# Performance work log

Measured on AMD Instinct MI355X. Metric: run time of the kernel, lower is better.

Reference implementation:

```python
import jax, jax.numpy as jnp
import numpy as np

EPS = 1e-05


def setup_inputs() -> dict:
    key = jax.random.key(0)
    k0, k1, k2, k3, k4 = jax.random.split(key, 5)
    B, N, D = 8, 4096, 1024
    scale = 1.0 / np.sqrt(D)  # roughly xavier scale for D x D
    return {
        "x": jax.random.normal(k0, (B, N, D), dtype=jnp.float32),
        "w_query_real": jax.random.normal(k1, (D, D), dtype=jnp.float32) * scale,
        "w_query_imag": jax.random.normal(k2, (D, D), dtype=jnp.float32) * scale,
        "w_key": jax.random.normal(k3, (D, D), dtype=jnp.float32) * scale,
        "w_value": jax.random.normal(k4, (D, D), dtype=jnp.float32) * scale,
    }


def reference(x, w_query_real, w_query_imag, w_key, w_value):
    # x is real -> x_real = x_imag = x (torch fallback branch)
    q_real = jnp.einsum('bnd,de->bne', x, w_query_real)
    q_imag = jnp.einsum('bnd,de->bne', x, w_query_imag)
    query = jax.nn.relu(q_real) * jax.nn.relu(q_imag)  # relu gating; dropout p=0

    key = jnp.einsum('bnd,de->bne', x, w_key)
    value = jnp.einsum('bnd,de->bne', x, w_value)
    # L2 norm over the sequence axis (dim=1), keepdim
    key = key / (jnp.linalg.norm(key, axis=1, keepdims=True) + EPS)
    value = value / (jnp.linalg.norm(value, axis=1, keepdims=True) + EPS)

    kv_attn = jax.nn.relu(jnp.einsum('bnd,bne->bde', key, value))  # [B, D, D]
    return jnp.einsum('bnd,bde->bne', query, kv_attn)
```

## Files before the change

### kernel.cpp

```cpp
#include <hip/hip_runtime.h>
#include <stdint.h>
#include <stddef.h>

#define D_ 1024
#define NSEQ_ 4096
#define BATCH_ 8
#define BN_ (BATCH_ * NSEQ_)

typedef __attribute__((ext_vector_type(8))) short short8;
typedef __attribute__((ext_vector_type(4))) short short4_t;
typedef __attribute__((ext_vector_type(4))) float float4_t;

__device__ __forceinline__ short f2b(float f) {
  union { float f; uint32_t u; } x; x.f = f;
  uint32_t r = x.u + 0x7fffu + ((x.u >> 16) & 1u);
  return (short)(r >> 16);
}
__device__ __forceinline__ float b2f(short s) {
  union { float f; uint32_t u; } x; x.u = ((uint32_t)(uint16_t)s) << 16; return x.f;
}

__device__ __forceinline__ void gll16(const void* g, void* l) {
  auto gp = reinterpret_cast<const uint32_t __attribute__((address_space(1)))*>(
      reinterpret_cast<uintptr_t>(g));
  auto lp = reinterpret_cast<uint32_t __attribute__((address_space(3)))*>(
      reinterpret_cast<uintptr_t>(l));
  __builtin_amdgcn_global_load_lds(gp, lp, 16, 0, 0);
}

#define MFMA16(a, b, c) __builtin_amdgcn_mfma_f32_16x16x32_bf16(a, b, c, 0, 0, 0)

__global__ void convert_x(const float* __restrict__ X, short* __restrict__ Xb) {
  const size_t i = (size_t)blockIdx.x * 256 + threadIdx.x;
  const float4_t* p = (const float4_t*)(X + i * 8);
  float4_t a = __builtin_nontemporal_load(p);
  float4_t b = __builtin_nontemporal_load(p + 1);
  short8 o;
  o[0] = f2b(a.x); o[1] = f2b(a.y); o[2] = f2b(a.z); o[3] = f2b(a.w);
  o[4] = f2b(b.x); o[5] = f2b(b.y); o[6] = f2b(b.z); o[7] = f2b(b.w);
  *(short8*)(Xb + i * 8) = o;
}

__global__ void transpose_convert_w(const float* __restrict__ w0, const float* __restrict__ w1,
                                    const float* __restrict__ w2, const float* __restrict__ w3,
                                    short* __restrict__ wT) {
  __shared__ float tile[32][33];
  const int z = blockIdx.z;
  const float* src = (z == 0) ? w0 : (z == 1) ? w1 : (z == 2) ? w2 : w3;
  const int d0 = blockIdx.y * 32, e0 = blockIdx.x * 32;
  const int tx = threadIdx.x, ty = threadIdx.y;
#pragma unroll
  for (int i = 0; i < 4; ++i) {
    int d = ty + i * 8;
    tile[d][tx] = __builtin_nontemporal_load(&src[(size_t)(d0 + d) * D_ + (e0 + tx)]);
  }
  __syncthreads();
#pragma unroll
  for (int i = 0; i < 4; ++i) {
    int e = ty + i * 8;
    const int eg = e0 + e;
    const int row = ((eg >> 4) << 6) + (z << 4) + (eg & 15);
    wT[(size_t)row * D_ + (d0 + tx)] = f2b(tile[tx][e]);
  }
}

__global__ __launch_bounds__(512, 2) void gemm_x4w(
    const short* __restrict__ Xb, const short* __restrict__ Wint,
    short* __restrict__ qout, short* __restrict__ kT, short* __restrict__ vT,
    float* __restrict__ ssk, float* __restrict__ ssv) {
  __shared__ short ring[4 * 16384];

  const int t = threadIdx.x;
  const int w = t >> 6;
  const int lane = t & 63;
  const int l16 = lane & 15;
  const int quad = lane >> 4;
  const int wm = w >> 2;
  const int wn = w & 3;

  const int bid = blockIdx.x;
  const int c = bid & 7;
  const int j = bid >> 3;
  const int ch = j >> 5;
  const int mtl = (ch & 1) * 8 + (j & 7);
  const int ntl = (ch >> 1) * 4 + ((j >> 3) & 3);
  const int mt = c * 16 + mtl;
  const int nt = ntl;
  const int M0 = mt * 256;
  const int N0 = nt * 256;
  const int E0 = nt * 64;

  const float4_t fz = {0.f, 0.f, 0.f, 0.f};
  float4_t acc[8][4];
#pragma unroll
  for (int i = 0; i < 8; ++i)
#pragma unroll
    for (int j2 = 0; j2 < 4; ++j2) acc[i][j2] = fz;

  size_t goffA[2], goffB[2];
  int ldsu[2];
#pragma unroll
  for (int r = 0; r < 2; ++r) {
    const int uu = w * 2 + r;
    const int row = uu * 16 + (lane >> 2);
    const int sp = (lane & 3) ^ ((row >> 1) & 3);
    goffA[r] = (size_t)(M0 + row) * 1024 + sp * 8;
    goffB[r] = (size_t)(N0 + row) * 1024 + sp * 8;
    ldsu[r] = uu * 512;
  }
  int aoff[8], boff[4];
#pragma unroll
  for (int i = 0; i < 8; ++i) {
    const int row = wm * 128 + i * 16 + l16;
    aoff[i] = row * 32 + ((quad ^ ((row >> 1) & 3)) << 3);
  }
#pragma unroll
  for (int j2 = 0; j2 < 4; ++j2) {
    const int row = wn * 64 + j2 * 16 + l16;
    boff[j2] = row * 32 + ((quad ^ ((row >> 1) & 3)) << 3);
  }

#pragma unroll
  for (int r = 0; r < 2; ++r) gll16(Xb + goffA[r], ring + ldsu[r]);
#pragma unroll
  for (int r = 0; r < 2; ++r) gll16(Wint + goffB[r], ring + 8192 + ldsu[r]);
#pragma unroll
  for (int r = 0; r < 2; ++r) gll16(Xb + goffA[r] + 32, ring + 16384 + ldsu[r]);
#pragma unroll
  for (int r = 0; r < 2; ++r) gll16(Wint + goffB[r] + 32, ring + 16384 + 8192 + ldsu[r]);
  asm volatile("s_waitcnt vmcnt(4)" ::: "memory");
  __builtin_amdgcn_s_barrier();

#pragma unroll 1
  for (int tt = 0; tt < 32; ++tt) {
    const short* As = ring + (tt & 3) * 16384;
    const short* Bs = As + 8192;
    short8 aF[8], bF[4];

#pragma unroll
    for (int i = 0; i < 4; ++i) aF[i] = *(const short8*)&As[aoff[i]];
#pragma unroll
    for (int j2 = 0; j2 < 4; ++j2) bF[j2] = *(const short8*)&Bs[boff[j2]];
    if (tt < 30) {
      short* dA = ring + ((tt + 2) & 3) * 16384;
      const int k0 = (tt + 2) * 32;
#pragma unroll
      for (int r = 0; r < 2; ++r) gll16(Xb + goffA[r] + k0, dA + ldsu[r]);
    }
    __builtin_amdgcn_s_barrier();
    asm volatile("s_waitcnt lgkmcnt(0)" ::: "memory");
    __builtin_amdgcn_s_setprio(1);
#pragma unroll
    for (int i = 0; i < 4; ++i)
#pragma unroll
      for (int j2 = 0; j2 < 4; ++j2) acc[i][j2] = MFMA16(aF[i], bF[j2], acc[i][j2]);
    __builtin_amdgcn_s_setprio(0);
    __builtin_amdgcn_s_barrier();

#pragma unroll
    for (int i = 4; i < 8; ++i) aF[i] = *(const short8*)&As[aoff[i]];
    if (tt < 30) {
      short* dB = ring + ((tt + 2) & 3) * 16384 + 8192;
      const int k0 = (tt + 2) * 32;
#pragma unroll
      for (int r = 0; r < 2; ++r) gll16(Wint + goffB[r] + k0, dB + ldsu[r]);
    }
    __builtin_amdgcn_s_barrier();
    asm volatile("s_waitcnt lgkmcnt(0)" ::: "memory");
    __builtin_amdgcn_s_setprio(1);
#pragma unroll
    for (int i = 4; i < 8; ++i)
#pragma unroll
      for (int j2 = 0; j2 < 4; ++j2) acc[i][j2] = MFMA16(aF[i], bF[j2], acc[i][j2]);
    __builtin_amdgcn_s_setprio(0);
    if (tt < 30) {
      asm volatile("s_waitcnt vmcnt(4)" ::: "memory");
    } else if (tt == 30) {
      asm volatile("s_waitcnt vmcnt(0)" ::: "memory");
    }
    __builtin_amdgcn_s_barrier();
  }

  const int e = E0 + wn * 16 + l16;
#pragma unroll
  for (int i = 0; i < 8; ++i) {
    const int rowg = M0 + wm * 128 + i * 16 + quad * 4;
#pragma unroll
    for (int rr = 0; rr < 4; ++rr) {
      float v = fmaxf(acc[i][0][rr], 0.f) * fmaxf(acc[i][1][rr], 0.f);
      qout[(size_t)(rowg + rr) * 1024 + e] = f2b(v);
    }
  }

  short* T = ring;
  const int b = M0 >> 12;
  const int n0 = M0 & 4095;
#pragma unroll
  for (int wt = 2; wt < 4; ++wt) {
    short* dst = (wt == 2) ? kT : vT;
    float* ss = (wt == 2) ? ssk : ssv;
    __syncthreads();
#pragma unroll
    for (int i = 0; i < 8; ++i) {
      const int nl = wm * 128 + i * 16 + quad * 4;
      const int el = wn * 16 + l16;
      short4_t pk;
#pragma unroll
      for (int rr = 0; rr < 4; ++rr) pk[rr] = f2b(acc[i][wt][rr]);
      *(short4_t*)&T[el * 264 + nl] = pk;
    }
    __syncthreads();
#pragma unroll
    for (int it = 0; it < 4; ++it) {
      const int ee = it * 16 + (t >> 5);
      const int nch = (t & 31) * 8;
      short8 vv = *(const short8*)&T[ee * 264 + nch];
      *(short8*)&dst[((size_t)b * 1024 + E0 + ee) * 4096 + n0 + nch] = vv;
      float s = 0.f;
#pragma unroll
      for (int x2 = 0; x2 < 8; ++x2) { float f = b2f(vv[x2]); s += f * f; }
      s += __shfl_xor(s, 1, 32);
      s += __shfl_xor(s, 2, 32);
      s += __shfl_xor(s, 4, 32);
      s += __shfl_xor(s, 8, 32);
      s += __shfl_xor(s, 16, 32);
      if ((t & 31) == 0) atomicAdd(&ss[b * 1024 + E0 + ee], s);
    }
  }
}

__global__ void finish_norms(const float* __restrict__ ss, float* __restrict__ inv) {
  const int i = blockIdx.x * 256 + threadIdx.x;
  if (i < 2 * BATCH_ * D_) inv[i] = 1.f / (sqrtf(ss[i]) + 1e-5f);
}

__global__ __launch_bounds__(256, 2) void gemm_bt(
    const short* __restrict__ A, const short* __restrict__ Bm,
    size_t sAb, size_t sBb, int K, int mode,
    const float* __restrict__ rsb, const float* __restrict__ csb,
    void* __restrict__ outp) {
  __shared__ short As[128 * 32];
  __shared__ short Bs[128 * 32];
  const int t = threadIdx.x;
  const int w = t >> 6;
  const int lane = t & 63;
  const int l16 = lane & 15;
  const int quad = lane >> 4;
  const int wm = w >> 1, wn = w & 1;
  const int M0 = blockIdx.y * 128, N0 = blockIdx.x * 128, b = blockIdx.z;
  const short* Ab = A + (size_t)b * sAb;
  const short* Bb = Bm + (size_t)b * sBb;

  const float4_t fz = {0.f, 0.f, 0.f, 0.f};
  float4_t acc[4][4];
#pragma unroll
  for (int i = 0; i < 4; ++i)
#pragma unroll
    for (int j = 0; j < 4; ++j) acc[i][j] = fz;

  const int rowq = lane >> 2;
  const int chunk = (lane & 3) * 8;

  for (int k0 = 0; k0 < K; k0 += 32) {
#pragma unroll
    for (int r = 0; r < 4; ++r) {
      const int q = w * 4 + r;
      if (q < 8) {
        const int row = q * 16 + rowq;
        gll16(Ab + (size_t)(M0 + row) * K + (k0 + chunk), &As[q * 512]);
      } else {
        const int row = (q - 8) * 16 + rowq;
        gll16(Bb + (size_t)(N0 + row) * K + (k0 + chunk), &Bs[(q - 8) * 512]);
      }
    }
    __syncthreads();
    short8 aF[4], bF[4];
#pragma unroll
    for (int i = 0; i < 4; ++i)
      aF[i] = *(const short8*)&As[(wm * 64 + i * 16 + l16) * 32 + quad * 8];
#pragma unroll
    for (int j = 0; j < 4; ++j)
      bF[j] = *(const short8*)&Bs[(wn * 64 + j * 16 + l16) * 32 + quad * 8];
#pragma unroll
    for (int i = 0; i < 4; ++i)
#pragma unroll
      for (int j = 0; j < 4; ++j) acc[i][j] = MFMA16(aF[i], bF[j], acc[i][j]);
    __syncthreads();
  }

  if (mode == 0) {
    short* ob = (short*)outp + (size_t)b * D_ * D_;
    const float* rs = rsb + b * D_ + M0;
    const float* cs = csb + b * D_ + N0;
#pragma unroll
    for (int i = 0; i < 4; ++i) {
      const int rl = wm * 64 + i * 16 + quad * 4;
#pragma unroll
      for (int j = 0; j < 4; ++j) {
        const int cl = wn * 64 + j * 16 + l16;
        const float csc = cs[cl];
#pragma unroll
        for (int rr = 0; rr < 4; ++rr) {
          float v = acc[i][j][rr] * rs[rl + rr] * csc;
          v = fmaxf(v, 0.f);
          ob[(size_t)(M0 + rl + rr) * 1024 + (N0 + cl)] = f2b(v);
        }
      }
    }
  } else {
    float* of = (float*)outp + (size_t)b * NSEQ_ * D_;
#pragma unroll
    for (int i = 0; i < 4; ++i) {
      const int rl = wm * 64 + i * 16 + quad * 4;
#pragma unroll
      for (int j = 0; j < 4; ++j) {
        const int cl = wn * 64 + j * 16 + l16;
#pragma unroll
        for (int rr = 0; rr < 4; ++rr)
          __builtin_nontemporal_store(acc[i][j][rr],
                                      &of[(size_t)(M0 + rl + rr) * 1024 + (N0 + cl)]);
      }
    }
  }
}

extern "C" void kernel_launch(void* const* d_in, const int* in_sizes, int n_in,
                              void* d_out, int out_size, void* d_ws, size_t ws_size,
                              hipStream_t stream) {
  const float* x = (const float*)d_in[0];
  const float* wqr = (const float*)d_in[1];
  const float* wqi = (const float*)d_in[2];
  const float* wk = (const float*)d_in[3];
  const float* wv = (const float*)d_in[4];

  short* wT = (short*)d_ws;
  short* qb = wT + (size_t)4 * D_ * D_;
  short* kT = qb + (size_t)BN_ * D_;
  short* vT = kT + (size_t)BATCH_ * D_ * NSEQ_;
  short* kvT = vT + (size_t)BATCH_ * D_ * NSEQ_;
  float* ssk = (float*)(kvT + (size_t)BATCH_ * D_ * D_);
  float* ssv = ssk + BATCH_ * D_;
  float* invk = ssv + BATCH_ * D_;
  float* invv = invk + BATCH_ * D_;

  short* xb = (short*)d_out;

  hipMemsetAsync(ssk, 0, (size_t)2 * BATCH_ * D_ * sizeof(float), stream);

  convert_x<<<dim3(16384), 256, 0, stream>>>(x, xb);

  transpose_convert_w<<<dim3(32, 32, 4), dim3(32, 8), 0, stream>>>(wqr, wqi, wk, wv, wT);

  gemm_x4w<<<dim3(2048), 512, 0, stream>>>(xb, wT, qb, kT, vT, ssk, ssv);

  finish_norms<<<dim3(64), 256, 0, stream>>>(ssk, invk);

  gemm_bt<<<dim3(8, 8, 8), 256, 0, stream>>>(
      vT, kT, (size_t)D_ * NSEQ_, (size_t)D_ * NSEQ_, 4096, 0, invv, invk, (void*)kvT);

  gemm_bt<<<dim3(8, 32, 8), 256, 0, stream>>>(
      qb, kvT, (size_t)NSEQ_ * D_, (size_t)D_ * D_, 1024, 1, nullptr, nullptr, d_out);
}
```

Before: 727.6 us.

## Pipeline batched GEMMs with a 4-stage LDS ring, swizzle and wider tiles

Replaces the simple synchronous gemm_bt with gemm_bt_p, which uses 512 threads and 128x256 tiles. It prefetches two K-steps ahead through a 4-buffer LDS ring with XOR swizzling, explicit vmcnt waits and s_setprio around the MFMAs. It also simplifies the block-to-tile mapping in gemm_x4w. The aim is to hide global load latency and LDS bank conflicts in the kv and output GEMMs. The cost is more LDS per block and more complex synchronisation. The tile remapping may also change L2 locality.

```diff
diff --git a/kernel.cpp b/kernel.cpp
--- a/kernel.cpp
+++ b/kernel.cpp
@@ -79,13 +79,9 @@
   const int wn = w & 3;
 
   const int bid = blockIdx.x;
-  const int c = bid & 7;
-  const int j = bid >> 3;
-  const int ch = j >> 5;
-  const int mtl = (ch & 1) * 8 + (j & 7);
-  const int ntl = (ch >> 1) * 4 + ((j >> 3) & 3);
-  const int mt = c * 16 + mtl;
-  const int nt = ntl;
+  const int lin = (bid & 7) * 256 + (bid >> 3);
+  const int mt = lin >> 4;
+  const int nt = lin & 15;
   const int M0 = mt * 256;
   const int N0 = nt * 256;
   const int E0 = nt * 64;
@@ -234,22 +230,24 @@
   if (i < 2 * BATCH_ * D_) inv[i] = 1.f / (sqrtf(ss[i]) + 1e-5f);
 }
 
-__global__ __launch_bounds__(256, 2) void gemm_bt(
+__global__ __launch_bounds__(512, 2) void gemm_bt_p(
     const short* __restrict__ A, const short* __restrict__ Bm,
     size_t sAb, size_t sBb, int K, int mode,
     const float* __restrict__ rsb, const float* __restrict__ csb,
     void* __restrict__ outp) {
-  __shared__ short As[128 * 32];
-  __shared__ short Bs[128 * 32];
+  __shared__ short ring[4 * 12288];
+
   const int t = threadIdx.x;
   const int w = t >> 6;
   const int lane = t & 63;
   const int l16 = lane & 15;
   const int quad = lane >> 4;
-  const int wm = w >> 1, wn = w & 1;
-  const int M0 = blockIdx.y * 128, N0 = blockIdx.x * 128, b = blockIdx.z;
+  const int wm = w >> 2;
+  const int wn = w & 3;
+  const int M0 = blockIdx.y * 128, N0 = blockIdx.x * 256, b = blockIdx.z;
   const short* Ab = A + (size_t)b * sAb;
   const short* Bb = Bm + (size_t)b * sBb;
+  const int NT = K >> 5;
 
   const float4_t fz = {0.f, 0.f, 0.f, 0.f};
   float4_t acc[4][4];
@@ -258,34 +256,63 @@
 #pragma unroll
     for (int j = 0; j < 4; ++j) acc[i][j] = fz;
 
-  const int rowq = lane >> 2;
-  const int chunk = (lane & 3) * 8;
-
-  for (int k0 = 0; k0 < K; k0 += 32) {
-#pragma unroll
-    for (int r = 0; r < 4; ++r) {
-      const int q = w * 4 + r;
-      if (q < 8) {
-        const int row = q * 16 + rowq;
-        gll16(Ab + (size_t)(M0 + row) * K + (k0 + chunk), &As[q * 512]);
-      } else {
-        const int row = (q - 8) * 16 + rowq;
-        gll16(Bb + (size_t)(N0 + row) * K + (k0 + chunk), &Bs[(q - 8) * 512]);
-      }
-    }
-    __syncthreads();
+  const short* gptr[3];
+  int ldso[3];
+#pragma unroll
+  for (int r = 0; r < 3; ++r) {
+    const int u = w * 3 + r;
+    const int lrow = (u < 8 ? u * 16 : (u - 8) * 16) + (lane >> 2);
+    const int sp = (lane & 3) ^ ((lrow >> 1) & 3);
+    gptr[r] = (u < 8 ? Ab + (size_t)(M0 + lrow) * K : Bb + (size_t)(N0 + lrow) * K) + sp * 8;
+    ldso[r] = (u < 8 ? u * 512 : 4096 + (u - 8) * 512);
+  }
+  int aoff[4], boff[4];
+#pragma unroll
+  for (int i = 0; i < 4; ++i) {
+    const int row = wm * 64 + i * 16 + l16;
+    aoff[i] = row * 32 + ((quad ^ ((row >> 1) & 3)) << 3);
+  }
+#pragma unroll
+  for (int j = 0; j < 4; ++j) {
+    const int row = wn * 64 + j * 16 + l16;
+    boff[j] = 4096 + row * 32 + ((quad ^ ((row >> 1) & 3)) << 3);
+  }
+
+#pragma unroll
+  for (int r = 0; r < 3; ++r) gll16(gptr[r], ring + ldso[r]);
+#pragma unroll
+  for (int r = 0; r < 3; ++r) gll16(gptr[r] + 32, ring + 12288 + ldso[r]);
+  asm volatile("s_waitcnt vmcnt(3)" ::: "memory");
+  __builtin_amdgcn_s_barrier();
+
+#pragma unroll 1
+  for (int tt = 0; tt < NT; ++tt) {
+    const short* As = ring + (tt & 3) * 12288;
     short8 aF[4], bF[4];
 #pragma unroll
+    for (int i = 0; i < 4; ++i) aF[i] = *(const short8*)&As[aoff[i]];
+#pragma unroll
+    for (int j = 0; j < 4; ++j) bF[j] = *(const short8*)&As[boff[j]];
+    if (tt < NT - 2) {
+      short* dS = ring + ((tt + 2) & 3) * 12288;
+      const int k0 = (tt + 2) * 32;
+#pragma unroll
+      for (int r = 0; r < 3; ++r) gll16(gptr[r] + k0, dS + ldso[r]);
+    }
+    __builtin_amdgcn_s_barrier();
+    asm volatile("s_waitcnt lgkmcnt(0)" ::: "memory");
+    __builtin_amdgcn_s_setprio(1);
+#pragma unroll
     for (int i = 0; i < 4; ++i)
-      aF[i] = *(const short8*)&As[(wm * 64 + i * 16 + l16) * 32 + quad * 8];
-#pragma unroll
-    for (int j = 0; j < 4; ++j)
-      bF[j] = *(const short8*)&Bs[(wn * 64 + j * 16 + l16) * 32 + quad * 8];
-#pragma unroll
-    for (int i = 0; i < 4; ++i)
 #pragma unroll
       for (int j = 0; j < 4; ++j) acc[i][j] = MFMA16(aF[i], bF[j], acc[i][j]);
-    __syncthreads();
+    __builtin_amdgcn_s_setprio(0);
+    if (tt < NT - 2) {
+      asm volatile("s_waitcnt vmcnt(3)" ::: "memory");
+    } else if (tt == NT - 2) {
+      asm volatile("s_waitcnt vmcnt(0)" ::: "memory");
+    }
+    __builtin_amdgcn_s_barrier();
   }
 
   if (mode == 0) {
@@ -355,9 +382,9 @@
 
   finish_norms<<<dim3(64), 256, 0, stream>>>(ssk, invk);
 
-  gemm_bt<<<dim3(8, 8, 8), 256, 0, stream>>>(
+  gemm_bt_p<<<dim3(4, 8, 8), 512, 0, stream>>>(
       vT, kT, (size_t)D_ * NSEQ_, (size_t)D_ * NSEQ_, 4096, 0, invv, invk, (void*)kvT);
 
-  gemm_bt<<<dim3(8, 32, 8), 256, 0, stream>>>(
+  gemm_bt_p<<<dim3(4, 32, 8), 512, 0, stream>>>(
       qb, kvT, (size_t)NSEQ_ * D_, (size_t)D_ * D_, 1024, 1, nullptr, nullptr, d_out);
 }
```

Measured after the change: 689.6 us. -5.2%, faster.
